# Optimization experiments

Measured on AMD Instinct MI355X. Metric: run time of the kernel, lower is better.

Reference implementation:

```python
import jax, jax.numpy as jnp
import numpy as np

CLASS_NUM = 80
K_DET = 300          # fixed per-image detection budget (jit-friendly stand-in for nonzero())
IOU_T = 0.3          # NMS IoU threshold from original code: nms(boxes_c, 0.3)


def setup_inputs() -> dict:
    key = jax.random.key(0)
    k1, k2, k3 = jax.random.split(key, 3)
    N, C = 64, 3 * (5 + CLASS_NUM)
    out13 = jax.random.normal(k1, (N, C, 13, 13), jnp.float32)
    out26 = jax.random.normal(k2, (N, C, 26, 26), jnp.float32)
    out52 = jax.random.normal(k3, (N, C, 52, 52), jnp.float32)
    # Standard YOLOv3 ANCHORS_GROUP (pixel units), keyed by grid size.
    anchors13 = jnp.array([[116., 90.], [156., 198.], [373., 326.]], jnp.float32)
    anchors26 = jnp.array([[30., 61.], [62., 45.], [59., 119.]], jnp.float32)
    anchors52 = jnp.array([[10., 13.], [16., 30.], [33., 23.]], jnp.float32)
    thresh = jnp.float32(2.5)
    return {"out13": out13, "out26": out26, "out52": out52,
            "anchors13": anchors13, "anchors26": anchors26, "anchors52": anchors52,
            "thresh": thresh}


def _decode(out, stride, anchor, thresh):
    # out: [N, 3*(5+CLS), H, W] -> boxes [N, H*W*3, 6] = (conf, ox, oy, w, h, cls)
    N, C, H, W = out.shape
    o = jnp.transpose(out, (0, 2, 3, 1)).reshape(N, H, W, 3, -1)
    conf = o[..., 0]
    gy = jnp.arange(H, dtype=o.dtype).reshape(1, H, 1, 1)
    gx = jnp.arange(W, dtype=o.dtype).reshape(1, 1, W, 1)
    ox = (gx + o[..., 1]) * stride          # ox = (w_idx + tx) * t
    oy = (gy + o[..., 2]) * stride          # oy = (h_idx + ty) * t
    w = jnp.exp(o[..., 3]) * anchor[:, 0]   # w = exp(tw) * anchor_w[a]
    h = jnp.exp(o[..., 4]) * anchor[:, 1]   # h = exp(th) * anchor_h[a]
    cls = jnp.argmax(o[..., 5:], axis=-1).astype(o.dtype)
    box = jnp.stack([conf, ox, oy, w, h, cls], axis=-1)
    return box.reshape(N, H * W * 3, 6), (conf > thresh).reshape(N, H * W * 3)


def _iou_matrix(c):
    # c: [K,4] corners (x1,y1,x2,y2) -> [K,K] pairwise IoU
    ix1 = jnp.maximum(c[:, None, 0], c[None, :, 0])
    iy1 = jnp.maximum(c[:, None, 1], c[None, :, 1])
    ix2 = jnp.minimum(c[:, None, 2], c[None, :, 2])
    iy2 = jnp.minimum(c[:, None, 3], c[None, :, 3])
    inter = jnp.clip(ix2 - ix1, 0) * jnp.clip(iy2 - iy1, 0)
    area = (c[:, 2] - c[:, 0]) * (c[:, 3] - c[:, 1])
    union = area[:, None] + area[None, :] - inter
    return inter / jnp.maximum(union, 1e-9)


def _nms_one(box6, valid):
    # box6: [K,6] sorted by conf desc; greedy per-class NMS -> keep mask [K]
    cx, cy, w, h = box6[:, 1], box6[:, 2], box6[:, 3], box6[:, 4]
    corners = jnp.stack([cx - w / 2, cy - h / 2, cx + w / 2, cy + h / 2], axis=-1)
    iou = _iou_matrix(corners)
    same_cls = box6[:, None, 5] == box6[None, :, 5]
    sup = (iou > IOU_T) & same_cls          # [K,K] suppression pairs
    K = valid.shape[0]
    def body(keep, i):
        k = valid[i] & jnp.logical_not(jnp.any(keep & sup[:, i]))
        return keep.at[i].set(k), None
    keep, _ = jax.lax.scan(body, jnp.zeros((K,), bool), jnp.arange(K))
    return keep


def _forward(out13, out26, out52, anchors13, anchors26, anchors52, thresh):
    b13, m13 = _decode(out13, 32.0, anchors13, thresh)
    b26, m26 = _decode(out26, 16.0, anchors26, thresh)
    b52, m52 = _decode(out52, 8.0, anchors52, thresh)
    box = jnp.concatenate([b13, b26, b52], axis=1)   # [N, M, 6], M=10647
    mask = jnp.concatenate([m13, m26, m52], axis=1)  # [N, M]
    N = box.shape[0]
    score = jnp.where(mask, box[..., 0], -jnp.inf)
    _, topi = jax.lax.top_k(score, K_DET)            # conf-descending per image
    sel = jnp.take_along_axis(box, topi[..., None], axis=1)   # [N, K, 6]
    valid = jnp.take_along_axis(mask, topi, axis=1)            # [N, K]
    keep = jax.vmap(_nms_one)(sel, valid)                      # [N, K]
    nidx = jnp.broadcast_to(jnp.arange(N, dtype=box.dtype)[:, None], keep.shape)
    dets = jnp.concatenate([sel, nidx[..., None]], axis=-1)    # [N, K, 7]
    return dets * keep.astype(box.dtype)[..., None]            # suppressed rows zeroed


def reference(out13, out26, out52, anchors13, anchors26, anchors52, thresh):
    return _forward(out13, out26, out52, anchors13, anchors26, anchors52, thresh)
```

## Files before the change

### kernel.cpp

```cpp
#include <hip/hip_runtime.h>

#define CAP  256
#define KDET 300
#define NW   4
#define BDIM 512

__global__ __launch_bounds__(BDIM) void yolo_fused_kernel(
        const float* __restrict__ o13, const float* __restrict__ o26,
        const float* __restrict__ o52,
        const float* __restrict__ a13, const float* __restrict__ a26,
        const float* __restrict__ a52,
        const float* __restrict__ thresh_p,
        float* __restrict__ out) {
    int n   = blockIdx.x;
    int tid = threadIdx.x;

    __shared__ int   l_cnt;
    __shared__ int   l_pack[CAP];
    __shared__ float l_conf[CAP];
    __shared__ float s_conf[CAP], s_cx[CAP], s_cy[CAP], s_w[CAP], s_h[CAP],
                     s_cls[CAP], s_idx[CAP];
    __shared__ float r_conf[CAP], r_cx[CAP], r_cy[CAP], r_w[CAP], r_h[CAP], r_cls[CAP];
    __shared__ float s_x1[CAP], s_y1[CAP], s_x2[CAP], s_y2[CAP];
    __shared__ unsigned long long sup[CAP][NW];
    __shared__ unsigned long long keepmask[NW];

    if (tid == 0) l_cnt = 0;
    __syncthreads();

    float thr = *thresh_p;

    for (int t = tid; t < 507; t += BDIM) {
        int a = t / 169, pix = t - a * 169;
        float conf = o13[((size_t)(n * 255 + a * 85)) * 169 + pix];
        if (conf > thr) {
            int slot = atomicAdd(&l_cnt, 1);
            if (slot < CAP) { l_pack[slot] = (0 << 16) | (a << 12) | pix; l_conf[slot] = conf; }
        }
    }
    for (int t = tid; t < 507; t += BDIM) {
        int a = t / 169, v = t - a * 169;
        const float4 c4 = *(const float4*)(o26 + ((size_t)(n * 255 + a * 85)) * 676 + v * 4);
        #pragma unroll
        for (int k = 0; k < 4; ++k) {
            float conf = (&c4.x)[k];
            if (conf > thr) {
                int slot = atomicAdd(&l_cnt, 1);
                if (slot < CAP) { l_pack[slot] = (1 << 16) | (a << 12) | (v * 4 + k); l_conf[slot] = conf; }
            }
        }
    }
    for (int t = tid; t < 2028; t += BDIM) {
        int a = t / 676, v = t - a * 676;
        const float4 c4 = *(const float4*)(o52 + ((size_t)(n * 255 + a * 85)) * 2704 + v * 4);
        #pragma unroll
        for (int k = 0; k < 4; ++k) {
            float conf = (&c4.x)[k];
            if (conf > thr) {
                int slot = atomicAdd(&l_cnt, 1);
                if (slot < CAP) { l_pack[slot] = (2 << 16) | (a << 12) | (v * 4 + k); l_conf[slot] = conf; }
            }
        }
    }
    __syncthreads();
    int cnt = l_cnt < CAP ? l_cnt : CAP;

    for (int i = tid; i < cnt; i += BDIM) {
        int pk  = l_pack[i];
        int s   = pk >> 16;
        int a   = (pk >> 12) & 0xF;
        int pix = pk & 0xFFF;
        const float* op = (s == 0) ? o13 : (s == 1) ? o26 : o52;
        const float* an = (s == 0) ? a13 : (s == 1) ? a26 : a52;
        int   HW     = (s == 0) ? 169 : (s == 1) ? 676 : 2704;
        int   W      = (s == 0) ? 13  : (s == 1) ? 26  : 52;
        float stride = (s == 0) ? 32.f : (s == 1) ? 16.f : 8.f;
        int   base   = (s == 0) ? 0   : (s == 1) ? 507 : 2535;

        const float* p = op + ((size_t)(n * 255 + a * 85)) * HW + pix;
        float o1 = p[(size_t)1 * HW];
        float o2 = p[(size_t)2 * HW];
        float o3 = p[(size_t)3 * HW];
        float o4 = p[(size_t)4 * HW];
        int gx = pix % W, gy = pix / W;
        float ox = ((float)gx + o1) * stride;
        float oy = ((float)gy + o2) * stride;
        float bw = expf(o3) * an[2 * a + 0];
        float bh = expf(o4) * an[2 * a + 1];

        float best = p[(size_t)5 * HW];
        int cls = 0;
        for (int c = 1; c < 80; ++c) {
            float v = p[(size_t)(5 + c) * HW];
            if (v > best) { best = v; cls = c; }
        }

        s_conf[i] = l_conf[i];
        s_cx[i] = ox; s_cy[i] = oy; s_w[i] = bw; s_h[i] = bh;
        s_cls[i] = (float)cls;
        s_idx[i] = (float)(base + pix * 3 + a);
    }
    __syncthreads();

    for (int i = tid; i < cnt; i += BDIM) {
        float ci = s_conf[i], ii = s_idx[i];
        int rank = 0;
        for (int j = 0; j < cnt; ++j) {
            float cj = s_conf[j];
            rank += (cj > ci) || (cj == ci && s_idx[j] < ii);
        }
        float cx = s_cx[i], cy = s_cy[i], w = s_w[i], h = s_h[i];
        r_conf[rank] = ci; r_cx[rank] = cx; r_cy[rank] = cy;
        r_w[rank] = w;     r_h[rank] = h;   r_cls[rank] = s_cls[i];
        s_x1[rank] = cx - 0.5f * w;
        s_y1[rank] = cy - 0.5f * h;
        s_x2[rank] = cx + 0.5f * w;
        s_y2[rank] = cy + 0.5f * h;
    }
    __syncthreads();

    int nwords = (cnt + 63) >> 6;
    int items  = cnt * nwords;
    for (int t = tid; t < items; t += BDIM) {
        int i  = t / nwords;
        int wi = t - i * nwords;
        float xi1 = s_x1[i], yi1 = s_y1[i], xi2 = s_x2[i], yi2 = s_y2[i];
        float cli = r_cls[i];
        float area_i = (xi2 - xi1) * (yi2 - yi1);
        unsigned long long m = 0;
        int jbase = wi << 6;
        for (int b = 0; b < 64; ++b) {
            int j = jbase + b;
            if (j >= cnt) break;
            if (j == i) continue;
            float xl = fmaxf(xi1, s_x1[j]);
            float yt = fmaxf(yi1, s_y1[j]);
            float xr = fminf(xi2, s_x2[j]);
            float yb = fminf(yi2, s_y2[j]);
            float inter  = fmaxf(xr - xl, 0.f) * fmaxf(yb - yt, 0.f);
            float area_j = (s_x2[j] - s_x1[j]) * (s_y2[j] - s_y1[j]);
            float iou    = inter / fmaxf(area_i + area_j - inter, 1e-9f);
            if (iou > 0.3f && cli == r_cls[j]) m |= (1ull << b);
        }
        sup[i][wi] = m;
    }
    __syncthreads();

    if (tid == 0) {
        unsigned long long km[NW];
        for (int w = 0; w < NW; ++w) km[w] = 0ull;
        for (int i = 0; i < cnt; ++i) {
            unsigned long long sbits = 0;
            for (int w = 0; w < nwords; ++w) sbits |= sup[i][w] & km[w];
            if (sbits == 0) km[i >> 6] |= (1ull << (i & 63));
        }
        for (int w = 0; w < NW; ++w) keepmask[w] = km[w];
    }
    __syncthreads();

    float* obase = out + (size_t)n * KDET * 7;
    float nf = (float)n;
    for (int t = tid; t < KDET * 7; t += BDIM) {
        int r = t / 7, c = t - r * 7;
        float v = 0.f;
        if (r < cnt && ((keepmask[r >> 6] >> (r & 63)) & 1ull)) {
            switch (c) {
                case 0: v = r_conf[r]; break;
                case 1: v = r_cx[r];   break;
                case 2: v = r_cy[r];   break;
                case 3: v = r_w[r];    break;
                case 4: v = r_h[r];    break;
                case 5: v = r_cls[r];  break;
                case 6: v = nf;        break;
            }
        }
        obase[t] = v;
    }
}

extern "C" void kernel_launch(void* const* d_in, const int* in_sizes, int n_in,
                              void* d_out, int out_size, void* d_ws, size_t ws_size,
                              hipStream_t stream) {
    const float* out13 = (const float*)d_in[0];
    const float* out26 = (const float*)d_in[1];
    const float* out52 = (const float*)d_in[2];
    const float* a13   = (const float*)d_in[3];
    const float* a26   = (const float*)d_in[4];
    const float* a52   = (const float*)d_in[5];
    const float* thr   = (const float*)d_in[6];
    float* out = (float*)d_out;

    int N = in_sizes[0] / (255 * 13 * 13);

    yolo_fused_kernel<<<N, BDIM, 0, stream>>>(out13, out26, out52,
                                              a13, a26, a52, thr, out);
}
```

Measured before the change: 305.3 us.

## Split fused per-image kernel into grid-wide scan/decode kernel and per-image NMS kernel

Replaces the single kernel, which ran one block per image, with two kernels. A grid-wide scan kernel assigns one thread per anchor cell across all images. It decodes boxes that pass the threshold, computes the argmax over the 80 classes, and appends each candidate to a per-image workspace buffer using a global atomic counter. A second kernel, one block per image, loads those candidates, rank-sorts them, builds the IoU suppression bitmask, runs the greedy NMS and writes the output. The aim is to use far more of the GPU during the memory-bound scan than 64 blocks can, at the cost of a memset, an extra launch and a global round trip for candidates; the old fused path remains as a fallback when the workspace is too small.

```diff
diff --git a/kernel.cpp b/kernel.cpp
--- a/kernel.cpp
+++ b/kernel.cpp
@@ -3,8 +3,169 @@
 #define CAP  256
 #define KDET 300
 #define NW   4
+#define SCAN_BDIM 256
+#define NMS_BDIM  256
+
+template<int HW, int W, int BASE>
+__device__ __forceinline__ void scan_one(int rem, float stride,
+        const float* __restrict__ op, const float* __restrict__ an,
+        float thr, int* __restrict__ counters, float* __restrict__ cand) {
+    int n   = rem / (3 * HW);
+    int q   = rem - n * (3 * HW);
+    int a   = q / HW;
+    int pix = q - a * HW;
+
+    const float* p = op + ((size_t)(n * 255 + a * 85)) * HW + pix;
+    float conf = p[0];
+    if (!(conf > thr)) return;
+
+    float o1 = p[(size_t)1 * HW];
+    float o2 = p[(size_t)2 * HW];
+    float o3 = p[(size_t)3 * HW];
+    float o4 = p[(size_t)4 * HW];
+    int gx = pix % W, gy = pix / W;
+    float ox = ((float)gx + o1) * stride;
+    float oy = ((float)gy + o2) * stride;
+    float bw = expf(o3) * an[2 * a + 0];
+    float bh = expf(o4) * an[2 * a + 1];
+
+    float best = p[(size_t)5 * HW];
+    int cls = 0;
+    #pragma unroll 4
+    for (int c = 1; c < 80; ++c) {
+        float v = p[(size_t)(5 + c) * HW];
+        if (v > best) { best = v; cls = c; }
+    }
+
+    int slot = atomicAdd(counters + n, 1);
+    if (slot < CAP) {
+        float4* w4 = (float4*)(cand + ((size_t)n * CAP + slot) * 8);
+        w4[0] = make_float4(conf, ox, oy, bw);
+        w4[1] = make_float4(bh, (float)cls, (float)(BASE + pix * 3 + a), 0.f);
+    }
+}
+
+__global__ __launch_bounds__(SCAN_BDIM) void yolo_scan_kernel(
+        const float* __restrict__ o13, const float* __restrict__ o26,
+        const float* __restrict__ o52,
+        const float* __restrict__ a13, const float* __restrict__ a26,
+        const float* __restrict__ a52,
+        const float* __restrict__ thresh_p, int N,
+        int* __restrict__ counters, float* __restrict__ cand) {
+    int t = blockIdx.x * SCAN_BDIM + threadIdx.x;
+    float thr = *thresh_p;
+    int R0 = N * 507;
+    int R1 = N * 2028;
+    int R2 = N * 8112;
+    if (t < R0) {
+        scan_one<169, 13, 0>(t, 32.f, o13, a13, thr, counters, cand);
+    } else if (t < R0 + R1) {
+        scan_one<676, 26, 507>(t - R0, 16.f, o26, a26, thr, counters, cand);
+    } else if (t < R0 + R1 + R2) {
+        scan_one<2704, 52, 2535>(t - R0 - R1, 8.f, o52, a52, thr, counters, cand);
+    }
+}
+
+__global__ __launch_bounds__(NMS_BDIM) void yolo_nms_kernel(
+        const int* __restrict__ counters, const float* __restrict__ cand,
+        float* __restrict__ out) {
+    int n = blockIdx.x, tid = threadIdx.x;
+
+    __shared__ float s_conf[CAP], s_cx[CAP], s_cy[CAP], s_w[CAP], s_h[CAP],
+                     s_cls[CAP], s_idx[CAP];
+    __shared__ float r_conf[CAP], r_cx[CAP], r_cy[CAP], r_w[CAP], r_h[CAP], r_cls[CAP];
+    __shared__ float s_x1[CAP], s_y1[CAP], s_x2[CAP], s_y2[CAP];
+    __shared__ unsigned long long sup[CAP][NW];
+    __shared__ unsigned long long keepmask[NW];
+
+    int cnt = counters[n];
+    cnt = cnt < CAP ? cnt : CAP;
+
+    for (int i = tid; i < cnt; i += NMS_BDIM) {
+        const float4* c4 = (const float4*)(cand + ((size_t)n * CAP + i) * 8);
+        float4 lo = c4[0], hi = c4[1];
+        s_conf[i] = lo.x; s_cx[i] = lo.y; s_cy[i] = lo.z; s_w[i] = lo.w;
+        s_h[i]   = hi.x; s_cls[i] = hi.y; s_idx[i] = hi.z;
+    }
+    __syncthreads();
+
+    for (int i = tid; i < cnt; i += NMS_BDIM) {
+        float ci = s_conf[i], ii = s_idx[i];
+        int rank = 0;
+        for (int j = 0; j < cnt; ++j) {
+            float cj = s_conf[j];
+            rank += (cj > ci) || (cj == ci && s_idx[j] < ii);
+        }
+        float cx = s_cx[i], cy = s_cy[i], w = s_w[i], h = s_h[i];
+        r_conf[rank] = ci; r_cx[rank] = cx; r_cy[rank] = cy;
+        r_w[rank] = w;     r_h[rank] = h;   r_cls[rank] = s_cls[i];
+        s_x1[rank] = cx - 0.5f * w;
+        s_y1[rank] = cy - 0.5f * h;
+        s_x2[rank] = cx + 0.5f * w;
+        s_y2[rank] = cy + 0.5f * h;
+    }
+    __syncthreads();
+
+    int nwords = (cnt + 63) >> 6;
+    for (int t = tid; t < cnt * NW; t += NMS_BDIM) {
+        int i  = t >> 2;
+        int wi = t & 3;
+        if (wi >= nwords) continue;
+        float xi1 = s_x1[i], yi1 = s_y1[i], xi2 = s_x2[i], yi2 = s_y2[i];
+        float cli = r_cls[i];
+        float area_i = (xi2 - xi1) * (yi2 - yi1);
+        unsigned long long m = 0;
+        int jbase = wi << 6;
+        for (int b = 0; b < 64; ++b) {
+            int j = jbase + b;
+            if (j >= cnt) break;
+            if (j == i) continue;
+            float xl = fmaxf(xi1, s_x1[j]);
+            float yt = fmaxf(yi1, s_y1[j]);
+            float xr = fminf(xi2, s_x2[j]);
+            float yb = fminf(yi2, s_y2[j]);
+            float inter  = fmaxf(xr - xl, 0.f) * fmaxf(yb - yt, 0.f);
+            float area_j = (s_x2[j] - s_x1[j]) * (s_y2[j] - s_y1[j]);
+            float iou    = inter / fmaxf(area_i + area_j - inter, 1e-9f);
+            if (iou > 0.3f && cli == r_cls[j]) m |= (1ull << b);
+        }
+        sup[i][wi] = m;
+    }
+    __syncthreads();
+
+    if (tid == 0) {
+        unsigned long long km[NW];
+        for (int w = 0; w < NW; ++w) km[w] = 0ull;
+        for (int i = 0; i < cnt; ++i) {
+            unsigned long long sbits = 0;
+            for (int w = 0; w < nwords; ++w) sbits |= sup[i][w] & km[w];
+            if (sbits == 0) km[i >> 6] |= (1ull << (i & 63));
+        }
+        for (int w = 0; w < NW; ++w) keepmask[w] = km[w];
+    }
+    __syncthreads();
+
+    float* obase = out + (size_t)n * KDET * 7;
+    float nf = (float)n;
+    for (int t = tid; t < KDET * 7; t += NMS_BDIM) {
+        int r = t / 7, c = t - r * 7;
+        float v = 0.f;
+        if (r < cnt && ((keepmask[r >> 6] >> (r & 63)) & 1ull)) {
+            switch (c) {
+                case 0: v = r_conf[r]; break;
+                case 1: v = r_cx[r];   break;
+                case 2: v = r_cy[r];   break;
+                case 3: v = r_w[r];    break;
+                case 4: v = r_h[r];    break;
+                case 5: v = r_cls[r];  break;
+                case 6: v = nf;        break;
+            }
+        }
+        obase[t] = v;
+    }
+}
+
 #define BDIM 512
-
 __global__ __launch_bounds__(BDIM) void yolo_fused_kernel(
         const float* __restrict__ o13, const float* __restrict__ o26,
         const float* __restrict__ o52,
@@ -192,6 +353,18 @@
 
     int N = in_sizes[0] / (255 * 13 * 13);
 
-    yolo_fused_kernel<<<N, BDIM, 0, stream>>>(out13, out26, out52,
-                                              a13, a26, a52, thr, out);
-}
+    size_t req = 256 + (size_t)N * CAP * 8 * sizeof(float);
+    if (d_ws != nullptr && ws_size >= req) {
+        int*   counters = (int*)d_ws;
+        float* cand     = (float*)((char*)d_ws + 256);
+        hipMemsetAsync(counters, 0, (size_t)N * sizeof(int), stream);
+        int total  = N * 10647;
+        int blocks = (total + SCAN_BDIM - 1) / SCAN_BDIM;
+        yolo_scan_kernel<<<blocks, SCAN_BDIM, 0, stream>>>(
+            out13, out26, out52, a13, a26, a52, thr, N, counters, cand);
+        yolo_nms_kernel<<<N, NMS_BDIM, 0, stream>>>(counters, cand, out);
+    } else {
+        yolo_fused_kernel<<<N, BDIM, 0, stream>>>(out13, out26, out52,
+                                                  a13, a26, a52, thr, out);
+    }
+}
```

Measured after the change: 335.9 us. +10.0%, slower.

## Split fused YOLO kernel into grid-wide scan/decode and per-image NMS kernels

Applied to the files above, without the earlier changes.

Replaces the single one-block-per-image kernel with three launches. A tiny kernel zeroes per-image counters. A grid-wide scan kernel gives each anchor cell its own thread, which tests confidence, decodes the box and argmaxes the class. Survivors are appended through a global atomic into a staging area inside the output buffer. A per-image NMS kernel then loads the candidates, ranks them, builds the suppression mask and writes the final rows. The aim is to spread the confidence scan and decode across the whole GPU instead of only 64 blocks. In exchange it adds two extra launches, global atomics and reuse of the output buffer as scratch, and lowers the candidate cap from 256 to 240.

```diff
diff --git a/kernel.cpp b/kernel.cpp
--- a/kernel.cpp
+++ b/kernel.cpp
@@ -1,23 +1,83 @@
 #include <hip/hip_runtime.h>
 
-#define CAP  256
-#define KDET 300
-#define NW   4
-#define BDIM 512
+#define CAP   240
+#define KDET  300
+#define OSTR  2100
+#define CNT_OFF 2096
+#define NW    4
+#define SCAN_BDIM 256
+#define NMS_BDIM  256
 
-__global__ __launch_bounds__(BDIM) void yolo_fused_kernel(
+__global__ void yolo_zero_kernel(float* __restrict__ out, int N) {
+    int n = threadIdx.x;
+    if (n < N) ((int*)out)[(size_t)n * OSTR + CNT_OFF] = 0;
+}
+
+template<int HW, int W, int BASE>
+__device__ __forceinline__ void scan_one(int rem, float stride,
+        const float* __restrict__ op, const float* __restrict__ an,
+        float thr, float* __restrict__ out) {
+    int n   = rem / (3 * HW);
+    int q   = rem - n * (3 * HW);
+    int a   = q / HW;
+    int pix = q - a * HW;
+
+    const float* p = op + ((size_t)(n * 255 + a * 85)) * HW + pix;
+    float conf = p[0];
+    if (!(conf > thr)) return;
+
+    float o1 = p[(size_t)1 * HW];
+    float o2 = p[(size_t)2 * HW];
+    float o3 = p[(size_t)3 * HW];
+    float o4 = p[(size_t)4 * HW];
+    int gx = pix % W, gy = pix / W;
+    float ox = ((float)gx + o1) * stride;
+    float oy = ((float)gy + o2) * stride;
+    float bw = expf(o3) * an[2 * a + 0];
+    float bh = expf(o4) * an[2 * a + 1];
+
+    float best = p[(size_t)5 * HW];
+    int cls = 0;
+    #pragma unroll 4
+    for (int c = 1; c < 80; ++c) {
+        float v = p[(size_t)(5 + c) * HW];
+        if (v > best) { best = v; cls = c; }
+    }
+
+    int* cntp = (int*)out + (size_t)n * OSTR + CNT_OFF;
+    int slot = atomicAdd(cntp, 1);
+    if (slot < CAP) {
+        float4* w4 = (float4*)(out + (size_t)n * OSTR + slot * 8);
+        w4[0] = make_float4(conf, ox, oy, bw);
+        w4[1] = make_float4(bh, (float)cls, (float)(BASE + pix * 3 + a), 0.f);
+    }
+}
+
+__global__ __launch_bounds__(SCAN_BDIM) void yolo_scan_kernel(
         const float* __restrict__ o13, const float* __restrict__ o26,
         const float* __restrict__ o52,
         const float* __restrict__ a13, const float* __restrict__ a26,
         const float* __restrict__ a52,
-        const float* __restrict__ thresh_p,
+        const float* __restrict__ thresh_p, int N,
         float* __restrict__ out) {
-    int n   = blockIdx.x;
-    int tid = threadIdx.x;
+    int t = blockIdx.x * SCAN_BDIM + threadIdx.x;
+    float thr = *thresh_p;
+    int R0 = N * 507;
+    int R1 = N * 2028;
+    int R2 = N * 8112;
+    if (t < R0) {
+        scan_one<169, 13, 0>(t, 32.f, o13, a13, thr, out);
+    } else if (t < R0 + R1) {
+        scan_one<676, 26, 507>(t - R0, 16.f, o26, a26, thr, out);
+    } else if (t < R0 + R1 + R2) {
+        scan_one<2704, 52, 2535>(t - R0 - R1, 8.f, o52, a52, thr, out);
+    }
+}
 
-    __shared__ int   l_cnt;
-    __shared__ int   l_pack[CAP];
-    __shared__ float l_conf[CAP];
+__global__ __launch_bounds__(NMS_BDIM) void yolo_nms_kernel(
+        float* __restrict__ out) {
+    int n = blockIdx.x, tid = threadIdx.x;
+
     __shared__ float s_conf[CAP], s_cx[CAP], s_cy[CAP], s_w[CAP], s_h[CAP],
                      s_cls[CAP], s_idx[CAP];
     __shared__ float r_conf[CAP], r_cx[CAP], r_cy[CAP], r_w[CAP], r_h[CAP], r_cls[CAP];
@@ -25,84 +85,19 @@
     __shared__ unsigned long long sup[CAP][NW];
     __shared__ unsigned long long keepmask[NW];
 
-    if (tid == 0) l_cnt = 0;
-    __syncthreads();
+    float* blk = out + (size_t)n * OSTR;
+    int cnt = ((const int*)out)[(size_t)n * OSTR + CNT_OFF];
+    cnt = cnt < CAP ? cnt : CAP;
 
-    float thr = *thresh_p;
-
-    for (int t = tid; t < 507; t += BDIM) {
-        int a = t / 169, pix = t - a * 169;
-        float conf = o13[((size_t)(n * 255 + a * 85)) * 169 + pix];
-        if (conf > thr) {
-            int slot = atomicAdd(&l_cnt, 1);
-            if (slot < CAP) { l_pack[slot] = (0 << 16) | (a << 12) | pix; l_conf[slot] = conf; }
-        }
-    }
-    for (int t = tid; t < 507; t += BDIM) {
-        int a = t / 169, v = t - a * 169;
-        const float4 c4 = *(const float4*)(o26 + ((size_t)(n * 255 + a * 85)) * 676 + v * 4);
-        #pragma unroll
-        for (int k = 0; k < 4; ++k) {
-            float conf = (&c4.x)[k];
-            if (conf > thr) {
-                int slot = atomicAdd(&l_cnt, 1);
-                if (slot < CAP) { l_pack[slot] = (1 << 16) | (a << 12) | (v * 4 + k); l_conf[slot] = conf; }
-            }
-        }
-    }
-    for (int t = tid; t < 2028; t += BDIM) {
-        int a = t / 676, v = t - a * 676;
-        const float4 c4 = *(const float4*)(o52 + ((size_t)(n * 255 + a * 85)) * 2704 + v * 4);
-        #pragma unroll
-        for (int k = 0; k < 4; ++k) {
-            float conf = (&c4.x)[k];
-            if (conf > thr) {
-                int slot = atomicAdd(&l_cnt, 1);
-                if (slot < CAP) { l_pack[slot] = (2 << 16) | (a << 12) | (v * 4 + k); l_conf[slot] = conf; }
-            }
-        }
-    }
-    __syncthreads();
-    int cnt = l_cnt < CAP ? l_cnt : CAP;
-
-    for (int i = tid; i < cnt; i += BDIM) {
-        int pk  = l_pack[i];
-        int s   = pk >> 16;
-        int a   = (pk >> 12) & 0xF;
-        int pix = pk & 0xFFF;
-        const float* op = (s == 0) ? o13 : (s == 1) ? o26 : o52;
-        const float* an = (s == 0) ? a13 : (s == 1) ? a26 : a52;
-        int   HW     = (s == 0) ? 169 : (s == 1) ? 676 : 2704;
-        int   W      = (s == 0) ? 13  : (s == 1) ? 26  : 52;
-        float stride = (s == 0) ? 32.f : (s == 1) ? 16.f : 8.f;
-        int   base   = (s == 0) ? 0   : (s == 1) ? 507 : 2535;
-
-        const float* p = op + ((size_t)(n * 255 + a * 85)) * HW + pix;
-        float o1 = p[(size_t)1 * HW];
-        float o2 = p[(size_t)2 * HW];
-        float o3 = p[(size_t)3 * HW];
-        float o4 = p[(size_t)4 * HW];
-        int gx = pix % W, gy = pix / W;
-        float ox = ((float)gx + o1) * stride;
-        float oy = ((float)gy + o2) * stride;
-        float bw = expf(o3) * an[2 * a + 0];
-        float bh = expf(o4) * an[2 * a + 1];
-
-        float best = p[(size_t)5 * HW];
-        int cls = 0;
-        for (int c = 1; c < 80; ++c) {
-            float v = p[(size_t)(5 + c) * HW];
-            if (v > best) { best = v; cls = c; }
-        }
-
-        s_conf[i] = l_conf[i];
-        s_cx[i] = ox; s_cy[i] = oy; s_w[i] = bw; s_h[i] = bh;
-        s_cls[i] = (float)cls;
-        s_idx[i] = (float)(base + pix * 3 + a);
+    for (int i = tid; i < cnt; i += NMS_BDIM) {
+        const float4* c4 = (const float4*)(blk + (size_t)i * 8);
+        float4 lo = c4[0], hi = c4[1];
+        s_conf[i] = lo.x; s_cx[i] = lo.y; s_cy[i] = lo.z; s_w[i] = lo.w;
+        s_h[i]   = hi.x; s_cls[i] = hi.y; s_idx[i] = hi.z;
     }
     __syncthreads();
 
-    for (int i = tid; i < cnt; i += BDIM) {
+    for (int i = tid; i < cnt; i += NMS_BDIM) {
         float ci = s_conf[i], ii = s_idx[i];
         int rank = 0;
         for (int j = 0; j < cnt; ++j) {
@@ -120,10 +115,10 @@
     __syncthreads();
 
     int nwords = (cnt + 63) >> 6;
-    int items  = cnt * nwords;
-    for (int t = tid; t < items; t += BDIM) {
-        int i  = t / nwords;
-        int wi = t - i * nwords;
+    for (int t = tid; t < cnt * NW; t += NMS_BDIM) {
+        int i  = t >> 2;
+        int wi = t & 3;
+        if (wi >= nwords) continue;
         float xi1 = s_x1[i], yi1 = s_y1[i], xi2 = s_x2[i], yi2 = s_y2[i];
         float cli = r_cls[i];
         float area_i = (xi2 - xi1) * (yi2 - yi1);
@@ -158,9 +153,8 @@
     }
     __syncthreads();
 
-    float* obase = out + (size_t)n * KDET * 7;
     float nf = (float)n;
-    for (int t = tid; t < KDET * 7; t += BDIM) {
+    for (int t = tid; t < KDET * 7; t += NMS_BDIM) {
         int r = t / 7, c = t - r * 7;
         float v = 0.f;
         if (r < cnt && ((keepmask[r >> 6] >> (r & 63)) & 1ull)) {
@@ -174,7 +168,7 @@
                 case 6: v = nf;        break;
             }
         }
-        obase[t] = v;
+        blk[t] = v;
     }
 }
 
@@ -192,6 +186,10 @@
 
     int N = in_sizes[0] / (255 * 13 * 13);
 
-    yolo_fused_kernel<<<N, BDIM, 0, stream>>>(out13, out26, out52,
-                                              a13, a26, a52, thr, out);
+    yolo_zero_kernel<<<1, 64, 0, stream>>>(out, N);
+    int total  = N * 10647;
+    int blocks = (total + SCAN_BDIM - 1) / SCAN_BDIM;
+    yolo_scan_kernel<<<blocks, SCAN_BDIM, 0, stream>>>(
+        out13, out26, out52, a13, a26, a52, thr, N, out);
+    yolo_nms_kernel<<<N, NMS_BDIM, 0, stream>>>(out);
 }
```

After: 320.2 us. 1.05x slower.

## Parallelize class argmax across 16-lane groups and NMS scan across a wavefront

Applied to the files above, without the earlier changes.

Doubles the block size to 1024 threads and splits each candidate's 80-class argmax across 16 lanes, with a shuffle reduction to pick the winner. The suppression-matrix loop now uses shift and mask indexing in place of division. The serial greedy NMS scan moves from a single thread reading shared memory to a 64-lane wavefront that holds the suppression rows in registers and broadcasts each keep decision with a shuffle. The goal is to cut the serial latency of the per-image argmax and NMS phases, at the cost of more register pressure and a larger block.

```diff
diff --git a/kernel.cpp b/kernel.cpp
--- a/kernel.cpp
+++ b/kernel.cpp
@@ -3,7 +3,7 @@
 #define CAP  256
 #define KDET 300
 #define NW   4
-#define BDIM 512
+#define BDIM 1024
 
 __global__ __launch_bounds__(BDIM) void yolo_fused_kernel(
         const float* __restrict__ o13, const float* __restrict__ o26,
@@ -65,40 +65,53 @@
     __syncthreads();
     int cnt = l_cnt < CAP ? l_cnt : CAP;
 
-    for (int i = tid; i < cnt; i += BDIM) {
-        int pk  = l_pack[i];
-        int s   = pk >> 16;
-        int a   = (pk >> 12) & 0xF;
-        int pix = pk & 0xFFF;
-        const float* op = (s == 0) ? o13 : (s == 1) ? o26 : o52;
-        const float* an = (s == 0) ? a13 : (s == 1) ? a26 : a52;
-        int   HW     = (s == 0) ? 169 : (s == 1) ? 676 : 2704;
-        int   W      = (s == 0) ? 13  : (s == 1) ? 26  : 52;
-        float stride = (s == 0) ? 32.f : (s == 1) ? 16.f : 8.f;
-        int   base   = (s == 0) ? 0   : (s == 1) ? 507 : 2535;
-
-        const float* p = op + ((size_t)(n * 255 + a * 85)) * HW + pix;
-        float o1 = p[(size_t)1 * HW];
-        float o2 = p[(size_t)2 * HW];
-        float o3 = p[(size_t)3 * HW];
-        float o4 = p[(size_t)4 * HW];
-        int gx = pix % W, gy = pix / W;
-        float ox = ((float)gx + o1) * stride;
-        float oy = ((float)gy + o2) * stride;
-        float bw = expf(o3) * an[2 * a + 0];
-        float bh = expf(o4) * an[2 * a + 1];
-
-        float best = p[(size_t)5 * HW];
-        int cls = 0;
-        for (int c = 1; c < 80; ++c) {
-            float v = p[(size_t)(5 + c) * HW];
-            if (v > best) { best = v; cls = c; }
-        }
-
-        s_conf[i] = l_conf[i];
-        s_cx[i] = ox; s_cy[i] = oy; s_w[i] = bw; s_h[i] = bh;
-        s_cls[i] = (float)cls;
-        s_idx[i] = (float)(base + pix * 3 + a);
+    {
+        int lane  = tid & 15;
+        int group = tid >> 4;
+        for (int i = group; i < cnt; i += (BDIM >> 4)) {
+            int pk  = l_pack[i];
+            int s   = pk >> 16;
+            int a   = (pk >> 12) & 0xF;
+            int pix = pk & 0xFFF;
+            const float* op = (s == 0) ? o13 : (s == 1) ? o26 : o52;
+            const float* an = (s == 0) ? a13 : (s == 1) ? a26 : a52;
+            int   HW     = (s == 0) ? 169 : (s == 1) ? 676 : 2704;
+            int   W      = (s == 0) ? 13  : (s == 1) ? 26  : 52;
+            float stride = (s == 0) ? 32.f : (s == 1) ? 16.f : 8.f;
+            int   base   = (s == 0) ? 0   : (s == 1) ? 507 : 2535;
+
+            const float* p = op + ((size_t)(n * 255 + a * 85)) * HW + pix;
+
+            float bestv = p[(size_t)(5 + lane) * HW];
+            int   bestc = lane;
+            #pragma unroll
+            for (int k = 1; k < 5; ++k) {
+                int c = lane + 16 * k;
+                float v = p[(size_t)(5 + c) * HW];
+                if (v > bestv) { bestv = v; bestc = c; }
+            }
+            #pragma unroll
+            for (int m = 8; m; m >>= 1) {
+                float ov = __shfl_xor(bestv, m, 16);
+                int   oc = __shfl_xor(bestc, m, 16);
+                if (ov > bestv || (ov == bestv && oc < bestc)) { bestv = ov; bestc = oc; }
+            }
+
+            if (lane == 0) {
+                float o1 = p[(size_t)1 * HW];
+                float o2 = p[(size_t)2 * HW];
+                float o3 = p[(size_t)3 * HW];
+                float o4 = p[(size_t)4 * HW];
+                int gx = pix % W, gy = pix / W;
+                s_conf[i] = l_conf[i];
+                s_cx[i] = ((float)gx + o1) * stride;
+                s_cy[i] = ((float)gy + o2) * stride;
+                s_w[i]  = expf(o3) * an[2 * a + 0];
+                s_h[i]  = expf(o4) * an[2 * a + 1];
+                s_cls[i] = (float)bestc;
+                s_idx[i] = (float)(base + pix * 3 + a);
+            }
+        }
     }
     __syncthreads();
 
@@ -120,10 +133,10 @@
     __syncthreads();
 
     int nwords = (cnt + 63) >> 6;
-    int items  = cnt * nwords;
-    for (int t = tid; t < items; t += BDIM) {
-        int i  = t / nwords;
-        int wi = t - i * nwords;
+    for (int t = tid; t < cnt * NW; t += BDIM) {
+        int i  = t >> 2;
+        int wi = t & 3;
+        if (wi >= nwords) continue;
         float xi1 = s_x1[i], yi1 = s_y1[i], xi2 = s_x2[i], yi2 = s_y2[i];
         float cli = r_cls[i];
         float area_i = (xi2 - xi1) * (yi2 - yi1);
@@ -146,15 +159,36 @@
     }
     __syncthreads();
 
-    if (tid == 0) {
-        unsigned long long km[NW];
-        for (int w = 0; w < NW; ++w) km[w] = 0ull;
+    if (tid < 64) {
+        unsigned long long rA[NW] = {0,0,0,0}, rB[NW] = {0,0,0,0},
+                           rC[NW] = {0,0,0,0}, rD[NW] = {0,0,0,0};
+        #pragma unroll
+        for (int w = 0; w < NW; ++w) {
+            if (w < nwords) {
+                if (tid       < cnt) rA[w] = sup[tid      ][w];
+                if (tid + 64  < cnt) rB[w] = sup[tid + 64 ][w];
+                if (tid + 128 < cnt) rC[w] = sup[tid + 128][w];
+                if (tid + 192 < cnt) rD[w] = sup[tid + 192][w];
+            }
+        }
+        unsigned long long km[NW] = {0,0,0,0};
         for (int i = 0; i < cnt; ++i) {
-            unsigned long long sbits = 0;
-            for (int w = 0; w < nwords; ++w) sbits |= sup[i][w] & km[w];
-            if (sbits == 0) km[i >> 6] |= (1ull << (i & 63));
-        }
-        for (int w = 0; w < NW; ++w) keepmask[w] = km[w];
+            int r = i >> 6;
+            unsigned long long sb;
+            switch (r) {
+                case 0:  sb = (rA[0]&km[0])|(rA[1]&km[1])|(rA[2]&km[2])|(rA[3]&km[3]); break;
+                case 1:  sb = (rB[0]&km[0])|(rB[1]&km[1])|(rB[2]&km[2])|(rB[3]&km[3]); break;
+                case 2:  sb = (rC[0]&km[0])|(rC[1]&km[1])|(rC[2]&km[2])|(rC[3]&km[3]); break;
+                default: sb = (rD[0]&km[0])|(rD[1]&km[1])|(rD[2]&km[2])|(rD[3]&km[3]); break;
+            }
+            int keep_i = (sb == 0ull) ? 1 : 0;
+            keep_i = __shfl(keep_i, i & 63);
+            if (keep_i) km[r] |= (1ull << (i & 63));
+        }
+        if (tid == 0) {
+            #pragma unroll
+            for (int w = 0; w < NW; ++w) keepmask[w] = km[w];
+        }
     }
     __syncthreads();
 
```

Measured after the change: 288.9 us. 1.06x faster.
